# Performance work log

Measured on AMD Instinct MI355X. Metric: run time of the kernel, lower is better.

## Reference

```python
import jax, jax.numpy as jnp
import numpy as np

N_HEADS = 16
ROPE = 64        # qk_rope_head_dim
KV_LORA = 512
V_DIM = 128
THETA = 10000.0

def rms_norm(x, w, eps=1e-6):
    return x * jax.lax.rsqrt(jnp.mean(x * x, axis=-1, keepdims=True) + eps) * w

def rope_cos_sin(T, d, theta=THETA):
    half = d // 2
    inv = 1.0 / theta ** (jnp.arange(half, dtype=jnp.float32) / half)
    ang = jnp.arange(T, dtype=jnp.float32)[:, None] * inv  # (T, half)
    return jnp.cos(ang), jnp.sin(ang)

def apply_rot(x, cos, sin):
    # x: (B,T,H,D); complex rotation on interleaved pairs
    xr, xi = x[..., 0::2], x[..., 1::2]
    c = cos[None, :, None, :]
    s = sin[None, :, None, :]
    orr = xr * c - xi * s
    oi = xr * s + xi * c
    return jnp.stack([orr, oi], axis=-1).reshape(x.shape)

def setup_inputs() -> dict:
    key = jax.random.key(0)
    ks = jax.random.split(key, 8)
    B, T, C = 2, 2048, 2048
    QLR = 1536
    x = jax.random.normal(ks[0], (B, T, C), dtype=jnp.float32)
    mask = jnp.tril(jnp.ones((T, T), dtype=jnp.int32))[None, None]
    sc = 0.02
    w_qa = jax.random.normal(ks[1], (QLR, C), dtype=jnp.float32) * sc
    qa_norm_w = jnp.ones((QLR,), dtype=jnp.float32)
    w_qb = jax.random.normal(ks[2], (N_HEADS * 2 * ROPE, QLR), dtype=jnp.float32) * sc
    w_kva = jax.random.normal(ks[3], (KV_LORA + ROPE, C), dtype=jnp.float32) * sc
    kva_norm_w = jnp.ones((KV_LORA,), dtype=jnp.float32)
    w_kvb = jax.random.normal(ks[4], (N_HEADS * (ROPE + V_DIM), KV_LORA), dtype=jnp.float32) * sc
    w_o = jax.random.normal(ks[5], (C, N_HEADS * V_DIM), dtype=jnp.float32) * sc
    return {"x": x, "mask": mask, "w_qa": w_qa, "qa_norm_w": qa_norm_w, "w_qb": w_qb,
            "w_kva": w_kva, "kva_norm_w": kva_norm_w, "w_kvb": w_kvb, "w_o": w_o}

def reference(x, mask, w_qa, qa_norm_w, w_qb, w_kva, kva_norm_w, w_kvb, w_o):
    B, T, C = x.shape
    # Q: low-rank compress -> norm -> up-project, split nope/rope halves
    q_c = rms_norm(x @ w_qa.T, qa_norm_w)
    q = (q_c @ w_qb.T).reshape(B, T, N_HEADS, 2 * ROPE)
    q_nope, q_rope = q[..., :ROPE], q[..., ROPE:]
    # KV: joint low-rank + shared rope key
    kv_a = x @ w_kva.T
    kv_c = rms_norm(kv_a[..., :KV_LORA], kva_norm_w)
    k_rope_raw = kv_a[..., KV_LORA:]                       # (B,T,ROPE)
    kv = (kv_c @ w_kvb.T).reshape(B, T, N_HEADS, ROPE + V_DIM)
    k_content, v = kv[..., :ROPE], kv[..., ROPE:]
    k_rope = jnp.broadcast_to(k_rope_raw[:, :, None, :], (B, T, N_HEADS, ROPE))
    cos, sin = rope_cos_sin(T, ROPE)
    q_rope = apply_rot(q_rope, cos, sin)
    k_rope = apply_rot(k_rope, cos, sin)
    q = jnp.concatenate([q_nope, q_rope], axis=-1)         # (B,T,H,2*ROPE)
    k = jnp.concatenate([k_content, k_rope], axis=-1)
    att = jnp.einsum('bqhd,bkhd->bhqk', q, k) * (ROPE ** -0.5)
    att = jnp.where(mask == 0, -jnp.inf, att)
    att = jax.nn.softmax(att, axis=-1)
    # source's nan-guard: uniform attention if any nan appeared
    att = jnp.where(jnp.any(jnp.isnan(att)), jnp.float32(1.0 / T), att)
    out = jnp.einsum('bhqk,bkhd->bqhd', att, v).reshape(B, T, N_HEADS * V_DIM)
    return out @ w_o.T
```

## Files before the change

### kernel.cpp

```cpp
#include <hip/hip_runtime.h>

typedef short bf16x8 __attribute__((ext_vector_type(8)));
typedef unsigned short u16x8 __attribute__((ext_vector_type(8)));
typedef unsigned short u16x4 __attribute__((ext_vector_type(4)));
typedef float f32x4 __attribute__((ext_vector_type(4)));
typedef unsigned u32x4 __attribute__((ext_vector_type(4)));
typedef unsigned u32x2 __attribute__((ext_vector_type(2)));

#define DEV static __device__ __forceinline__

DEV float bf2f(unsigned short u) { return __uint_as_float(((unsigned)u) << 16); }
DEV unsigned short f2bf(float f) {
  unsigned u = __float_as_uint(f);
  return (unsigned short)((u + 0x7fffu + ((u >> 16) & 1u)) >> 16);
}
DEV unsigned cvtpk(float lo, float hi) {
  unsigned r;
  asm("v_cvt_pk_bf16_f32 %0, %1, %2" : "=v"(r) : "v"(lo), "v"(hi));
  return r;
}
DEV void p32swap(unsigned& a, unsigned& b) {
  asm volatile("v_permlane32_swap_b32 %0, %1" : "+v"(a), "+v"(b));
}
DEV void p16swap(unsigned& a, unsigned& b) {
  asm volatile("v_permlane16_swap_b32 %0, %1" : "+v"(a), "+v"(b));
}

#define GLDS16(g, l)                                                                   \
  __builtin_amdgcn_global_load_lds((const __attribute__((address_space(1))) void*)(g), \
                                   (__attribute__((address_space(3))) void*)(l), 16, 0, 0)

DEV void cvt_body(const float* __restrict__ src, unsigned short* __restrict__ dst,
                  int rows, int cols, int dstRows, int bid) {
  int i = bid * 256 + (int)threadIdx.x;
  int e = i << 2;
  int r = e / cols;
  int c = e - r * cols;
  u16x4 o = {0, 0, 0, 0};
  if (r < rows) {
    const float* p = src + (size_t)r * cols + c;
    o[0] = f2bf(p[0]); o[1] = f2bf(p[1]); o[2] = f2bf(p[2]); o[3] = f2bf(p[3]);
  }
  *(u16x4*)(dst + e) = o;
}

__global__ __launch_bounds__(256) void convert_all(
    const float* __restrict__ x, const float* __restrict__ w_qa, const float* __restrict__ w_kva,
    const float* __restrict__ w_qb, const float* __restrict__ w_kvb, const float* __restrict__ w_o,
    unsigned short* __restrict__ xb, unsigned short* __restrict__ wqkva,
    unsigned short* __restrict__ wqbb, unsigned short* __restrict__ wkvbb,
    unsigned short* __restrict__ wob) {
  int bid = blockIdx.x;
  if (bid < 8192)        cvt_body(x,     xb,                        4096, 2048, 4096, bid);
  else if (bid < 11264)  cvt_body(w_qa,  wqkva,                     1536, 2048, 1536, bid - 8192);
  else if (bid < 12544)  cvt_body(w_kva, wqkva + (size_t)1536*2048,  576, 2048,  640, bid - 11264);
  else if (bid < 15616)  cvt_body(w_qb,  wqbb,                      2048, 1536, 2048, bid - 12544);
  else if (bid < 17152)  cvt_body(w_kvb, wkvbb,                     3072,  512, 3072, bid - 15616);
  else                   cvt_body(w_o,   wob,                       2048, 2048, 2048, bid - 17152);
}

template <typename OutT>
__global__ __launch_bounds__(256, 2) void gemm_bt(const unsigned short* __restrict__ A,
                                                  const unsigned short* __restrict__ B,
                                                  OutT* __restrict__ C, int M, int N, int K) {
  __shared__ __align__(16) unsigned short As[128 * 64];
  __shared__ __align__(16) unsigned short Bs[128 * 64];
  const int tid = threadIdx.x;
  const int lane = tid & 63, wave = tid >> 6;
  const int l16 = lane & 15, lhi = lane >> 4;
  const int nbn = N >> 7;
  const int bm = blockIdx.x / nbn, bn = blockIdx.x - bm * nbn;
  const int m0 = bm << 7, n0 = bn << 7;
  const int wm = (wave >> 1) << 6, wn = (wave & 1) << 6;
  f32x4 acc[4][4] = {};
  for (int k0 = 0; k0 < K; k0 += 64) {
#pragma unroll
    for (int it = 0; it < 4; ++it) {
      int slot = it * 256 + tid;
      int row = slot >> 3, col = (slot & 7) << 3;
      GLDS16(A + (size_t)(m0 + row) * K + k0 + col, As + (it * 256 + wave * 64) * 8);
      GLDS16(B + (size_t)(n0 + row) * K + k0 + col, Bs + (it * 256 + wave * 64) * 8);
    }
    __syncthreads();
#pragma unroll
    for (int ks = 0; ks < 2; ++ks) {
      bf16x8 a[4], b[4];
#pragma unroll
      for (int i = 0; i < 4; ++i) {
        a[i] = *(const bf16x8*)(As + (wm + i * 16 + l16) * 64 + ks * 32 + lhi * 8);
        b[i] = *(const bf16x8*)(Bs + (wn + i * 16 + l16) * 64 + ks * 32 + lhi * 8);
      }
#pragma unroll
      for (int i = 0; i < 4; ++i)
#pragma unroll
        for (int j = 0; j < 4; ++j)
          acc[i][j] = __builtin_amdgcn_mfma_f32_16x16x32_bf16(a[i], b[j], acc[i][j], 0, 0, 0);
    }
    __syncthreads();
  }
#pragma unroll
  for (int i = 0; i < 4; ++i)
#pragma unroll
    for (int j = 0; j < 4; ++j)
#pragma unroll
      for (int r = 0; r < 4; ++r) {
        int row = m0 + wm + i * 16 + lhi * 4 + r;
        int col = n0 + wn + j * 16 + l16;
        float v = acc[i][j][r];
        if constexpr (sizeof(OutT) == 4)
          C[(size_t)row * N + col] = v;
        else
          C[(size_t)row * N + col] = (OutT)f2bf(v);
      }
}

__global__ __launch_bounds__(256) void rms_fused(const unsigned short* __restrict__ qkva,
                                                 const float* __restrict__ qw,
                                                 const float* __restrict__ kvw,
                                                 unsigned short* __restrict__ q_c,
                                                 unsigned short* __restrict__ kv_c,
                                                 unsigned short* __restrict__ krope) {
  const int row = blockIdx.x, tid = threadIdx.x;
  const unsigned short* p = qkva + (size_t)row * 2176;
  float fq[8];
  float ssq = 0.f;
  const bool act = tid < 192;
  if (act) {
    u16x8 v = *(const u16x8*)(p + tid * 8);
#pragma unroll
    for (int j = 0; j < 8; ++j) { fq[j] = bf2f(v[j]); ssq += fq[j] * fq[j]; }
  }
  float f0 = bf2f(p[1536 + tid * 2]), f1 = bf2f(p[1536 + tid * 2 + 1]);
  float sskv = f0 * f0 + f1 * f1;
#pragma unroll
  for (int m = 1; m <= 32; m <<= 1) {
    ssq += __shfl_xor(ssq, m);
    sskv += __shfl_xor(sskv, m);
  }
  __shared__ float rq[4], rkv[4];
  if ((tid & 63) == 0) { rq[tid >> 6] = ssq; rkv[tid >> 6] = sskv; }
  __syncthreads();
  float rstdq = rsqrtf((rq[0] + rq[1] + rq[2] + rq[3]) * (1.f / 1536.f) + 1e-6f);
  float rstdkv = rsqrtf((rkv[0] + rkv[1] + rkv[2] + rkv[3]) * (1.f / 512.f) + 1e-6f);
  if (act) {
    u16x8 o;
#pragma unroll
    for (int j = 0; j < 8; ++j) o[j] = f2bf(fq[j] * rstdq * qw[tid * 8 + j]);
    *(u16x8*)(q_c + (size_t)row * 1536 + tid * 8) = o;
  }
  kv_c[(size_t)row * 512 + tid * 2]     = f2bf(f0 * rstdkv * kvw[tid * 2]);
  kv_c[(size_t)row * 512 + tid * 2 + 1] = f2bf(f1 * rstdkv * kvw[tid * 2 + 1]);
  if (tid < 32) {
    int j = tid;
    float xr = bf2f(p[2048 + 2 * j]), xi = bf2f(p[2048 + 2 * j + 1]);
    int t = row & 2047;
    float ang = (float)t * powf(10000.f, -(float)j * (1.f / 32.f));
    float c = cosf(ang), s = sinf(ang);
    krope[(size_t)row * 64 + 2 * j]     = f2bf(xr * c - xi * s);
    krope[(size_t)row * 64 + 2 * j + 1] = f2bf(xr * s + xi * c);
  }
}

__global__ __launch_bounds__(256) void v_transpose(const unsigned short* __restrict__ kvfull,
                                                   unsigned short* __restrict__ VT) {
  __shared__ unsigned short tile[64][137];
  const int tid = threadIdx.x;
  const int tt = blockIdx.x & 31, h = (blockIdx.x >> 5) & 15, b = blockIdx.x >> 9;
  const int t0 = tt * 64;
#pragma unroll
  for (int it = 0; it < 4; ++it) {
    int s = it * 256 + tid;
    int r = s >> 4, c = (s & 15) << 3;
    u16x8 v = *(const u16x8*)(kvfull + (size_t)(b * 2048 + t0 + r) * 3072 + h * 192 + 64 + c);
    *(u16x8*)(&tile[r][c]) = v;
  }
  __syncthreads();
#pragma unroll
  for (int it = 0; it < 4; ++it) {
    int s = it * 256 + tid;
    int d = s >> 3, tc = (s & 7) << 3;
    u16x8 o;
#pragma unroll
    for (int j = 0; j < 8; ++j) o[j] = tile[tc + j][d];
    *(u16x8*)(VT + ((size_t)(b * 16 + h) * 128 + d) * 2048 + t0 + tc) = o;
  }
}

__global__ __launch_bounds__(256, 2) void flash_attn(const unsigned short* __restrict__ qfull,
                                                     const unsigned short* __restrict__ kvfull,
                                                     const unsigned short* __restrict__ krope,
                                                     const unsigned short* __restrict__ Vt,
                                                     unsigned short* __restrict__ out) {
  const int tid = threadIdx.x, lane = tid & 63, wave = tid >> 6;
  const int l16 = lane & 15, lhi = lane >> 4;
  const int bid = blockIdx.x;
  const int vid = (bid & 7) * 64 + (bid >> 3);
  const int pr = vid & 15;
  const int h = (vid >> 4) & 15;
  const int b = vid >> 8;
  const int sA = pr, sB = 31 - pr;
  __shared__ __align__(16) unsigned short Ks[2][64 * 128];
  __shared__ __align__(16) unsigned short Vs[2][64 * 128];

  const float QSCALE = 0.125f * 1.44269504089f;
  bf16x8 qf[2][4];
  float m_run[2], l_run[2];
  int qrow_g[2];
  f32x4 o_acc[2][8] = {};
#pragma unroll
  for (int u = 0; u < 2; ++u) {
    const int s_u = u ? sB : sA;
    int t = s_u * 64 + wave * 16 + l16;
    qrow_g[u] = t;
    const unsigned short* qrow = qfull + (size_t)(b * 2048 + t) * 2048 + h * 128;
#pragma unroll
    for (int ks = 0; ks < 4; ++ks) {
      u16x8 raw = *(const u16x8*)(qrow + ks * 32 + lhi * 8);
      float f[8];
#pragma unroll
      for (int j = 0; j < 8; ++j) f[j] = bf2f(raw[j]);
      if (ks >= 2) {
#pragma unroll
        for (int pp = 0; pp < 4; ++pp) {
          int d = ks * 32 + lhi * 8 + 2 * pp;
          int jl = (d - 64) >> 1;
          float ang = (float)t * powf(10000.f, -(float)jl * (1.f / 32.f));
          float c = cosf(ang), s = sinf(ang);
          float xr = f[2 * pp], xi = f[2 * pp + 1];
          f[2 * pp] = xr * c - xi * s;
          f[2 * pp + 1] = xr * s + xi * c;
        }
      }
      bf16x8 fr;
#pragma unroll
      for (int j = 0; j < 8; ++j) fr[j] = (short)f2bf(f[j] * QSCALE);
      qf[u][ks] = fr;
    }
    m_run[u] = -1e30f;
    l_run[u] = 0.f;
  }

  const int bT = b * 2048;
  const unsigned short* Vbh = Vt + (size_t)(b * 16 + h) * 128 * 2048;

  auto stageK = [&](int kt, int buf) {
#pragma unroll
    for (int it = 0; it < 4; ++it) {
      int L = it * 4096 + wave * 1024 + lane * 16;
      int r = L >> 8;
      int w = (L & 255) ^ ((r & 7) << 4);
      int c = w >> 1;
      int tl = bT + kt * 64 + r;
      const unsigned short* src = (c < 64) ? kvfull + (size_t)tl * 3072 + h * 192 + c
                                           : krope + (size_t)tl * 64 + (c - 64);
      GLDS16(src, &Ks[buf][(it * 4096 + wave * 1024) >> 1]);
    }
  };
  auto stageV = [&](int kt, int buf) {
#pragma unroll
    for (int it = 0; it < 4; ++it) {
      int L = it * 4096 + wave * 1024 + lane * 16;
      int d = L >> 7;
      int w = (L & 127) ^ ((d & 7) << 4);
      GLDS16(Vbh + (size_t)d * 2048 + kt * 64 + (w >> 1), &Vs[buf][(it * 4096 + wave * 1024) >> 1]);
    }
  };

  stageK(0, 0);
  stageV(0, 0);
  __syncthreads();
  int cur = 0;

  for (int kt = 0; kt <= sB; ++kt) {
    if (kt < sB) { stageK(kt + 1, cur ^ 1); stageV(kt + 1, cur ^ 1); }
    const unsigned short* Kb = Ks[cur];
    const unsigned short* Vb = Vs[cur];
    const bool actA = (kt <= sA);

    f32x4 st[2][4] = {};
    __builtin_amdgcn_s_setprio(1);
#pragma unroll
    for (int ks = 0; ks < 4; ++ks) {
      bf16x8 kf[4];
#pragma unroll
      for (int nt = 0; nt < 4; ++nt) {
        int row = nt * 16 + l16;
        int byteoff = row * 256 + ((ks * 64 + lhi * 16) ^ ((l16 & 7) << 4));
        kf[nt] = *(const bf16x8*)((const char*)Kb + byteoff);
      }
#pragma unroll
      for (int u = 0; u < 2; ++u) {
        if (u == 0 && !actA) continue;
#pragma unroll
        for (int nt = 0; nt < 4; ++nt)
          st[u][nt] = __builtin_amdgcn_mfma_f32_16x16x32_bf16(kf[nt], qf[u][ks], st[u][nt], 0, 0, 0);
      }
    }
    __builtin_amdgcn_s_setprio(0);

    bf16x8 pw[2][2];
#pragma unroll
    for (int u = 0; u < 2; ++u) {
      if (u == 0 && !actA) continue;
      const int s_u = u ? sB : sA;
      if (kt == s_u) {
#pragma unroll
        for (int nt = 0; nt < 4; ++nt)
#pragma unroll
          for (int r = 0; r < 4; ++r) {
            int kg = kt * 64 + nt * 16 + lhi * 4 + r;
            st[u][nt][r] = (kg <= qrow_g[u]) ? st[u][nt][r] : -1e30f;
          }
      }
      float mx = -1e30f;
#pragma unroll
      for (int nt = 0; nt < 4; ++nt)
#pragma unroll
        for (int r = 0; r < 4; ++r) mx = fmaxf(mx, st[u][nt][r]);
      mx = fmaxf(mx, __shfl_xor(mx, 16));
      mx = fmaxf(mx, __shfl_xor(mx, 32));
      if (__ballot(mx > m_run[u] + 8.f)) {
        float mnew = fmaxf(m_run[u], mx);
        float sc = exp2f(m_run[u] - mnew);
        m_run[u] = mnew;
        l_run[u] *= sc;
#pragma unroll
        for (int dt = 0; dt < 8; ++dt) o_acc[u][dt] *= sc;
      }
      const float mcur = m_run[u];
      float sum = 0.f;
#pragma unroll
      for (int nt = 0; nt < 4; ++nt)
#pragma unroll
        for (int r = 0; r < 4; ++r) {
          float p = exp2f(st[u][nt][r] - mcur);
          st[u][nt][r] = p;
          sum += p;
        }
      sum += __shfl_xor(sum, 16);
      sum += __shfl_xor(sum, 32);
      l_run[u] += sum;
      unsigned pk01[4], pk23[4];
#pragma unroll
      for (int nt = 0; nt < 4; ++nt) {
        pk01[nt] = cvtpk(st[u][nt][0], st[u][nt][1]);
        pk23[nt] = cvtpk(st[u][nt][2], st[u][nt][3]);
      }
#pragma unroll
      for (int k2 = 0; k2 < 2; ++k2) {
        unsigned a0 = pk01[2 * k2], b0 = pk01[2 * k2 + 1];
        unsigned a1 = pk23[2 * k2], b1 = pk23[2 * k2 + 1];
        p32swap(a0, b0); p16swap(a0, b0);
        p32swap(a1, b1); p16swap(a1, b1);
        u32x4 t4 = {a0, a1, b0, b1};
        pw[u][k2] = *(bf16x8*)&t4;
      }
    }

    __builtin_amdgcn_s_setprio(1);
#pragma unroll
    for (int k2 = 0; k2 < 2; ++k2)
#pragma unroll
      for (int dt = 0; dt < 8; ++dt) {
        int row = dt * 16 + l16;
        int byteoff = row * 128 + ((k2 * 64 + lhi * 16) ^ ((l16 & 7) << 4));
        bf16x8 vf = *(const bf16x8*)((const char*)Vb + byteoff);
#pragma unroll
        for (int u = 0; u < 2; ++u) {
          if (u == 0 && !actA) continue;
          o_acc[u][dt] = __builtin_amdgcn_mfma_f32_16x16x32_bf16(vf, pw[u][k2], o_acc[u][dt], 0, 0, 0);
        }
      }
    __builtin_amdgcn_s_setprio(0);

    __syncthreads();
    cur ^= 1;
  }

#pragma unroll
  for (int u = 0; u < 2; ++u) {
    float inv = 1.0f / l_run[u];
    unsigned short* orow = out + (size_t)(b * 2048 + qrow_g[u]) * 2048 + h * 128;
#pragma unroll
    for (int dt = 0; dt < 8; ++dt) {
      unsigned w01 = cvtpk(o_acc[u][dt][0] * inv, o_acc[u][dt][1] * inv);
      unsigned w23 = cvtpk(o_acc[u][dt][2] * inv, o_acc[u][dt][3] * inv);
      u32x2 st2 = {w01, w23};
      *(u32x2*)(orow + dt * 16 + lhi * 4) = st2;
    }
  }
}

extern "C" void kernel_launch(void* const* d_in, const int* in_sizes, int n_in,
                              void* d_out, int out_size, void* d_ws, size_t ws_size,
                              hipStream_t stream) {
  (void)in_sizes; (void)n_in; (void)out_size; (void)ws_size;
  const float* x      = (const float*)d_in[0];
  const float* w_qa   = (const float*)d_in[2];
  const float* qa_nw  = (const float*)d_in[3];
  const float* w_qb   = (const float*)d_in[4];
  const float* w_kva  = (const float*)d_in[5];
  const float* kva_nw = (const float*)d_in[6];
  const float* w_kvb  = (const float*)d_in[7];
  const float* w_o    = (const float*)d_in[8];
  float* out = (float*)d_out;
  char* ws = (char*)d_ws;

  unsigned short* xb     = (unsigned short*)(ws + 0);
  unsigned short* wqkva  = (unsigned short*)(ws + 16777216);
  unsigned short* wqbb   = (unsigned short*)(ws + 25690112);
  unsigned short* wkvbb  = (unsigned short*)(ws + 31981568);
  unsigned short* wob    = (unsigned short*)(ws + 35127296);
  unsigned short* qkva   = (unsigned short*)(ws + 43515904);
  unsigned short* qfull  = (unsigned short*)(ws + 43515904);
  unsigned short* q_c    = (unsigned short*)(ws + 61341696);
  unsigned short* kv_c   = (unsigned short*)(ws + 73924608);
  unsigned short* krope  = (unsigned short*)(ws + 78118912);
  unsigned short* attno  = (unsigned short*)(ws + 61341696);
  unsigned short* Vattn  = (unsigned short*)(ws + 78643200);
  unsigned short* kvfull = (unsigned short*)d_out;

  convert_all<<<21248, 256, 0, stream>>>(x, w_qa, w_kva, w_qb, w_kvb, w_o,
                                         xb, wqkva, wqbb, wkvbb, wob);

  gemm_bt<unsigned short><<<32 * 17, 256, 0, stream>>>(xb, wqkva, qkva, 4096, 2176, 2048);

  rms_fused<<<4096, 256, 0, stream>>>(qkva, qa_nw, kva_nw, q_c, kv_c, krope);

  gemm_bt<unsigned short><<<32 * 16, 256, 0, stream>>>(q_c,  wqbb,  qfull,  4096, 2048, 1536);
  gemm_bt<unsigned short><<<32 * 24, 256, 0, stream>>>(kv_c, wkvbb, kvfull, 4096, 3072,  512);

  v_transpose<<<1024, 256, 0, stream>>>(kvfull, Vattn);

  flash_attn<<<512, 256, 0, stream>>>(qfull, kvfull, krope, Vattn, attno);

  gemm_bt<float><<<32 * 16, 256, 0, stream>>>(attno, wob, out, 4096, 2048, 2048);
}
```

Before: 286.6 us.

## Fuse V transpose into kv_b GEMM epilogue and restructure flash attention blocks

Adds a dedicated kv_b GEMM whose epilogue writes the K-content columns to kvfull and the V columns directly in transposed layout, removing the separate v_transpose kernel. Flash attention now gives each block a single 64-row query tile instead of a paired causal tile, with a head-major XCD mapping and alternating tile order for balance. The launch grows to 1024 blocks, shared memory is single-buffered, and launch bounds rise to 4 per SIMD. This drops the prefetch double-buffering, so each iteration waits on its loads behind a barrier, and the transposed V stores are narrow 8-byte strided writes.

```diff
diff --git a/kernel.cpp b/kernel.cpp
--- a/kernel.cpp
+++ b/kernel.cpp
@@ -114,6 +114,69 @@
       }
 }
 
+__global__ __launch_bounds__(256, 2) void gemm_kvb(const unsigned short* __restrict__ A,
+                                                   const unsigned short* __restrict__ B,
+                                                   unsigned short* __restrict__ kvfull,
+                                                   unsigned short* __restrict__ VT) {
+  const int M = 4096, N = 3072, K = 512;
+  __shared__ __align__(16) unsigned short As[128 * 64];
+  __shared__ __align__(16) unsigned short Bs[128 * 64];
+  const int tid = threadIdx.x;
+  const int lane = tid & 63, wave = tid >> 6;
+  const int l16 = lane & 15, lhi = lane >> 4;
+  const int nbn = N >> 7;
+  const int bm = blockIdx.x / nbn, bn = blockIdx.x - bm * nbn;
+  const int m0 = bm << 7, n0 = bn << 7;
+  const int wm = (wave >> 1) << 6, wn = (wave & 1) << 6;
+  f32x4 acc[4][4] = {};
+  for (int k0 = 0; k0 < K; k0 += 64) {
+#pragma unroll
+    for (int it = 0; it < 4; ++it) {
+      int slot = it * 256 + tid;
+      int row = slot >> 3, col = (slot & 7) << 3;
+      GLDS16(A + (size_t)(m0 + row) * K + k0 + col, As + (it * 256 + wave * 64) * 8);
+      GLDS16(B + (size_t)(n0 + row) * K + k0 + col, Bs + (it * 256 + wave * 64) * 8);
+    }
+    __syncthreads();
+#pragma unroll
+    for (int ks = 0; ks < 2; ++ks) {
+      bf16x8 a[4], b[4];
+#pragma unroll
+      for (int i = 0; i < 4; ++i) {
+        a[i] = *(const bf16x8*)(As + (wm + i * 16 + l16) * 64 + ks * 32 + lhi * 8);
+        b[i] = *(const bf16x8*)(Bs + (wn + i * 16 + l16) * 64 + ks * 32 + lhi * 8);
+      }
+#pragma unroll
+      for (int i = 0; i < 4; ++i)
+#pragma unroll
+        for (int j = 0; j < 4; ++j)
+          acc[i][j] = __builtin_amdgcn_mfma_f32_16x16x32_bf16(a[i], b[j], acc[i][j], 0, 0, 0);
+    }
+    __syncthreads();
+  }
+#pragma unroll
+  for (int i = 0; i < 4; ++i)
+#pragma unroll
+    for (int j = 0; j < 4; ++j) {
+      int col = n0 + wn + j * 16 + l16;
+      int h = col / 192;
+      int jc = col - h * 192;
+      int row0 = m0 + wm + i * 16 + lhi * 4;
+      if (jc < 64) {
+#pragma unroll
+        for (int r = 0; r < 4; ++r)
+          kvfull[(size_t)(row0 + r) * 3072 + col] = f2bf(acc[i][j][r]);
+      } else {
+        int d = jc - 64;
+        int b = row0 >> 11, t0 = row0 & 2047;
+        u16x4 pk;
+#pragma unroll
+        for (int r = 0; r < 4; ++r) pk[r] = f2bf(acc[i][j][r]);
+        *(u16x4*)(VT + ((size_t)((b * 16 + h) * 128 + d)) * 2048 + t0) = pk;
+      }
+    }
+}
+
 __global__ __launch_bounds__(256) void rms_fused(const unsigned short* __restrict__ qkva,
                                                  const float* __restrict__ qw,
                                                  const float* __restrict__ kvw,
@@ -161,32 +224,7 @@
   }
 }
 
-__global__ __launch_bounds__(256) void v_transpose(const unsigned short* __restrict__ kvfull,
-                                                   unsigned short* __restrict__ VT) {
-  __shared__ unsigned short tile[64][137];
-  const int tid = threadIdx.x;
-  const int tt = blockIdx.x & 31, h = (blockIdx.x >> 5) & 15, b = blockIdx.x >> 9;
-  const int t0 = tt * 64;
-#pragma unroll
-  for (int it = 0; it < 4; ++it) {
-    int s = it * 256 + tid;
-    int r = s >> 4, c = (s & 15) << 3;
-    u16x8 v = *(const u16x8*)(kvfull + (size_t)(b * 2048 + t0 + r) * 3072 + h * 192 + 64 + c);
-    *(u16x8*)(&tile[r][c]) = v;
-  }
-  __syncthreads();
-#pragma unroll
-  for (int it = 0; it < 4; ++it) {
-    int s = it * 256 + tid;
-    int d = s >> 3, tc = (s & 7) << 3;
-    u16x8 o;
-#pragma unroll
-    for (int j = 0; j < 8; ++j) o[j] = tile[tc + j][d];
-    *(u16x8*)(VT + ((size_t)(b * 16 + h) * 128 + d) * 2048 + t0 + tc) = o;
-  }
-}
-
-__global__ __launch_bounds__(256, 2) void flash_attn(const unsigned short* __restrict__ qfull,
+__global__ __launch_bounds__(256, 4) void flash_attn(const unsigned short* __restrict__ qfull,
                                                      const unsigned short* __restrict__ kvfull,
                                                      const unsigned short* __restrict__ krope,
                                                      const unsigned short* __restrict__ Vt,
@@ -194,25 +232,20 @@
   const int tid = threadIdx.x, lane = tid & 63, wave = tid >> 6;
   const int l16 = lane & 15, lhi = lane >> 4;
   const int bid = blockIdx.x;
-  const int vid = (bid & 7) * 64 + (bid >> 3);
-  const int pr = vid & 15;
-  const int h = (vid >> 4) & 15;
-  const int b = vid >> 8;
-  const int sA = pr, sB = 31 - pr;
-  __shared__ __align__(16) unsigned short Ks[2][64 * 128];
-  __shared__ __align__(16) unsigned short Vs[2][64 * 128];
+  const int xcd = bid & 7, Lb = bid >> 3;
+  const int bhl = Lb >> 5, cL = Lb & 31;
+  const int s = (bhl & 1) ? (31 - cL) : cL;
+  const int bh = xcd * 4 + bhl;
+  const int h = bh & 15, b = bh >> 4;
+  __shared__ __align__(16) unsigned short Ks[64 * 128];
+  __shared__ __align__(16) unsigned short Vs[64 * 128];
 
   const float QSCALE = 0.125f * 1.44269504089f;
-  bf16x8 qf[2][4];
-  float m_run[2], l_run[2];
-  int qrow_g[2];
-  f32x4 o_acc[2][8] = {};
-#pragma unroll
-  for (int u = 0; u < 2; ++u) {
-    const int s_u = u ? sB : sA;
-    int t = s_u * 64 + wave * 16 + l16;
-    qrow_g[u] = t;
-    const unsigned short* qrow = qfull + (size_t)(b * 2048 + t) * 2048 + h * 128;
+  bf16x8 qf[4];
+  f32x4 o_acc[8] = {};
+  const int qg = s * 64 + wave * 16 + l16;
+  {
+    const unsigned short* qrow = qfull + (size_t)(b * 2048 + qg) * 2048 + h * 128;
 #pragma unroll
     for (int ks = 0; ks < 4; ++ks) {
       u16x8 raw = *(const u16x8*)(qrow + ks * 32 + lhi * 8);
@@ -224,127 +257,104 @@
         for (int pp = 0; pp < 4; ++pp) {
           int d = ks * 32 + lhi * 8 + 2 * pp;
           int jl = (d - 64) >> 1;
-          float ang = (float)t * powf(10000.f, -(float)jl * (1.f / 32.f));
-          float c = cosf(ang), s = sinf(ang);
+          float ang = (float)qg * powf(10000.f, -(float)jl * (1.f / 32.f));
+          float co = cosf(ang), si = sinf(ang);
           float xr = f[2 * pp], xi = f[2 * pp + 1];
-          f[2 * pp] = xr * c - xi * s;
-          f[2 * pp + 1] = xr * s + xi * c;
+          f[2 * pp] = xr * co - xi * si;
+          f[2 * pp + 1] = xr * si + xi * co;
         }
       }
       bf16x8 fr;
 #pragma unroll
       for (int j = 0; j < 8; ++j) fr[j] = (short)f2bf(f[j] * QSCALE);
-      qf[u][ks] = fr;
-    }
-    m_run[u] = -1e30f;
-    l_run[u] = 0.f;
-  }
+      qf[ks] = fr;
+    }
+  }
+  float m_run = -1e30f, l_run = 0.f;
 
   const int bT = b * 2048;
   const unsigned short* Vbh = Vt + (size_t)(b * 16 + h) * 128 * 2048;
 
-  auto stageK = [&](int kt, int buf) {
+  for (int kt = 0; kt <= s; ++kt) {
 #pragma unroll
     for (int it = 0; it < 4; ++it) {
-      int L = it * 4096 + wave * 1024 + lane * 16;
-      int r = L >> 8;
-      int w = (L & 255) ^ ((r & 7) << 4);
-      int c = w >> 1;
+      int Lo = it * 4096 + wave * 1024 + lane * 16;
+      int r = Lo >> 8;
+      int w = (Lo & 255) ^ ((r & 7) << 4);
+      int cc = w >> 1;
       int tl = bT + kt * 64 + r;
-      const unsigned short* src = (c < 64) ? kvfull + (size_t)tl * 3072 + h * 192 + c
-                                           : krope + (size_t)tl * 64 + (c - 64);
-      GLDS16(src, &Ks[buf][(it * 4096 + wave * 1024) >> 1]);
-    }
-  };
-  auto stageV = [&](int kt, int buf) {
+      const unsigned short* src = (cc < 64) ? kvfull + (size_t)tl * 3072 + h * 192 + cc
+                                            : krope + (size_t)tl * 64 + (cc - 64);
+      GLDS16(src, Ks + ((it * 4096 + wave * 1024) >> 1));
+    }
 #pragma unroll
     for (int it = 0; it < 4; ++it) {
-      int L = it * 4096 + wave * 1024 + lane * 16;
-      int d = L >> 7;
-      int w = (L & 127) ^ ((d & 7) << 4);
-      GLDS16(Vbh + (size_t)d * 2048 + kt * 64 + (w >> 1), &Vs[buf][(it * 4096 + wave * 1024) >> 1]);
-    }
-  };
-
-  stageK(0, 0);
-  stageV(0, 0);
-  __syncthreads();
-  int cur = 0;
-
-  for (int kt = 0; kt <= sB; ++kt) {
-    if (kt < sB) { stageK(kt + 1, cur ^ 1); stageV(kt + 1, cur ^ 1); }
-    const unsigned short* Kb = Ks[cur];
-    const unsigned short* Vb = Vs[cur];
-    const bool actA = (kt <= sA);
-
-    f32x4 st[2][4] = {};
+      int Lo = it * 4096 + wave * 1024 + lane * 16;
+      int d = Lo >> 7;
+      int w = (Lo & 127) ^ ((d & 7) << 4);
+      GLDS16(Vbh + (size_t)d * 2048 + kt * 64 + (w >> 1), Vs + ((it * 4096 + wave * 1024) >> 1));
+    }
+    __syncthreads();
+
+    f32x4 st[4] = {};
     __builtin_amdgcn_s_setprio(1);
 #pragma unroll
     for (int ks = 0; ks < 4; ++ks) {
-      bf16x8 kf[4];
+      bf16x8 kf;
 #pragma unroll
       for (int nt = 0; nt < 4; ++nt) {
         int row = nt * 16 + l16;
         int byteoff = row * 256 + ((ks * 64 + lhi * 16) ^ ((l16 & 7) << 4));
-        kf[nt] = *(const bf16x8*)((const char*)Kb + byteoff);
-      }
-#pragma unroll
-      for (int u = 0; u < 2; ++u) {
-        if (u == 0 && !actA) continue;
-#pragma unroll
-        for (int nt = 0; nt < 4; ++nt)
-          st[u][nt] = __builtin_amdgcn_mfma_f32_16x16x32_bf16(kf[nt], qf[u][ks], st[u][nt], 0, 0, 0);
+        kf = *(const bf16x8*)((const char*)Ks + byteoff);
+        st[nt] = __builtin_amdgcn_mfma_f32_16x16x32_bf16(kf, qf[ks], st[nt], 0, 0, 0);
       }
     }
     __builtin_amdgcn_s_setprio(0);
 
-    bf16x8 pw[2][2];
-#pragma unroll
-    for (int u = 0; u < 2; ++u) {
-      if (u == 0 && !actA) continue;
-      const int s_u = u ? sB : sA;
-      if (kt == s_u) {
-#pragma unroll
-        for (int nt = 0; nt < 4; ++nt)
-#pragma unroll
-          for (int r = 0; r < 4; ++r) {
-            int kg = kt * 64 + nt * 16 + lhi * 4 + r;
-            st[u][nt][r] = (kg <= qrow_g[u]) ? st[u][nt][r] : -1e30f;
-          }
-      }
-      float mx = -1e30f;
+    if (kt == s) {
 #pragma unroll
       for (int nt = 0; nt < 4; ++nt)
 #pragma unroll
-        for (int r = 0; r < 4; ++r) mx = fmaxf(mx, st[u][nt][r]);
-      mx = fmaxf(mx, __shfl_xor(mx, 16));
-      mx = fmaxf(mx, __shfl_xor(mx, 32));
-      if (__ballot(mx > m_run[u] + 8.f)) {
-        float mnew = fmaxf(m_run[u], mx);
-        float sc = exp2f(m_run[u] - mnew);
-        m_run[u] = mnew;
-        l_run[u] *= sc;
-#pragma unroll
-        for (int dt = 0; dt < 8; ++dt) o_acc[u][dt] *= sc;
-      }
-      const float mcur = m_run[u];
-      float sum = 0.f;
-#pragma unroll
-      for (int nt = 0; nt < 4; ++nt)
-#pragma unroll
         for (int r = 0; r < 4; ++r) {
-          float p = exp2f(st[u][nt][r] - mcur);
-          st[u][nt][r] = p;
-          sum += p;
+          int kg = kt * 64 + nt * 16 + lhi * 4 + r;
+          st[nt][r] = (kg <= qg) ? st[nt][r] : -1e30f;
         }
-      sum += __shfl_xor(sum, 16);
-      sum += __shfl_xor(sum, 32);
-      l_run[u] += sum;
+    }
+    float mx = -1e30f;
+#pragma unroll
+    for (int nt = 0; nt < 4; ++nt)
+#pragma unroll
+      for (int r = 0; r < 4; ++r) mx = fmaxf(mx, st[nt][r]);
+    mx = fmaxf(mx, __shfl_xor(mx, 16));
+    mx = fmaxf(mx, __shfl_xor(mx, 32));
+    if (__ballot(mx > m_run + 8.f)) {
+      float mnew = fmaxf(m_run, mx);
+      float sc = exp2f(m_run - mnew);
+      m_run = mnew;
+      l_run *= sc;
+#pragma unroll
+      for (int dt = 0; dt < 8; ++dt) o_acc[dt] *= sc;
+    }
+    const float mcur = m_run;
+    float sum = 0.f;
+#pragma unroll
+    for (int nt = 0; nt < 4; ++nt)
+#pragma unroll
+      for (int r = 0; r < 4; ++r) {
+        float p = exp2f(st[nt][r] - mcur);
+        st[nt][r] = p;
+        sum += p;
+      }
+    sum += __shfl_xor(sum, 16);
+    sum += __shfl_xor(sum, 32);
+    l_run += sum;
+    bf16x8 pw[2];
+    {
       unsigned pk01[4], pk23[4];
 #pragma unroll
       for (int nt = 0; nt < 4; ++nt) {
-        pk01[nt] = cvtpk(st[u][nt][0], st[u][nt][1]);
-        pk23[nt] = cvtpk(st[u][nt][2], st[u][nt][3]);
+        pk01[nt] = cvtpk(st[nt][0], st[nt][1]);
+        pk23[nt] = cvtpk(st[nt][2], st[nt][3]);
       }
 #pragma unroll
       for (int k2 = 0; k2 < 2; ++k2) {
@@ -353,7 +363,7 @@
         p32swap(a0, b0); p16swap(a0, b0);
         p32swap(a1, b1); p16swap(a1, b1);
         u32x4 t4 = {a0, a1, b0, b1};
-        pw[u][k2] = *(bf16x8*)&t4;
+        pw[k2] = *(bf16x8*)&t4;
       }
     }
 
@@ -364,27 +374,21 @@
       for (int dt = 0; dt < 8; ++dt) {
         int row = dt * 16 + l16;
         int byteoff = row * 128 + ((k2 * 64 + lhi * 16) ^ ((l16 & 7) << 4));
-        bf16x8 vf = *(const bf16x8*)((const char*)Vb + byteoff);
-#pragma unroll
-        for (int u = 0; u < 2; ++u) {
-          if (u == 0 && !actA) continue;
-          o_acc[u][dt] = __builtin_amdgcn_mfma_f32_16x16x32_bf16(vf, pw[u][k2], o_acc[u][dt], 0, 0, 0);
-        }
+        bf16x8 vf = *(const bf16x8*)((const char*)Vs + byteoff);
+        o_acc[dt] = __builtin_amdgcn_mfma_f32_16x16x32_bf16(vf, pw[k2], o_acc[dt], 0, 0, 0);
       }
     __builtin_amdgcn_s_setprio(0);
 
     __syncthreads();
-    cur ^= 1;
-  }
-
-#pragma unroll
-  for (int u = 0; u < 2; ++u) {
-    float inv = 1.0f / l_run[u];
-    unsigned short* orow = out + (size_t)(b * 2048 + qrow_g[u]) * 2048 + h * 128;
+  }
+
+  {
+    float inv = 1.0f / l_run;
+    unsigned short* orow = out + (size_t)(b * 2048 + qg) * 2048 + h * 128;
 #pragma unroll
     for (int dt = 0; dt < 8; ++dt) {
-      unsigned w01 = cvtpk(o_acc[u][dt][0] * inv, o_acc[u][dt][1] * inv);
-      unsigned w23 = cvtpk(o_acc[u][dt][2] * inv, o_acc[u][dt][3] * inv);
+      unsigned w01 = cvtpk(o_acc[dt][0] * inv, o_acc[dt][1] * inv);
+      unsigned w23 = cvtpk(o_acc[dt][2] * inv, o_acc[dt][3] * inv);
       u32x2 st2 = {w01, w23};
       *(u32x2*)(orow + dt * 16 + lhi * 4) = st2;
     }
@@ -427,12 +431,10 @@
 
   rms_fused<<<4096, 256, 0, stream>>>(qkva, qa_nw, kva_nw, q_c, kv_c, krope);
 
-  gemm_bt<unsigned short><<<32 * 16, 256, 0, stream>>>(q_c,  wqbb,  qfull,  4096, 2048, 1536);
-  gemm_bt<unsigned short><<<32 * 24, 256, 0, stream>>>(kv_c, wkvbb, kvfull, 4096, 3072,  512);
-
-  v_transpose<<<1024, 256, 0, stream>>>(kvfull, Vattn);
-
-  flash_attn<<<512, 256, 0, stream>>>(qfull, kvfull, krope, Vattn, attno);
+  gemm_bt<unsigned short><<<32 * 16, 256, 0, stream>>>(q_c, wqbb, qfull, 4096, 2048, 1536);
+  gemm_kvb<<<32 * 24, 256, 0, stream>>>(kv_c, wkvbb, kvfull, Vattn);
+
+  flash_attn<<<1024, 256, 0, stream>>>(qfull, kvfull, krope, Vattn, attno);
 
   gemm_bt<float><<<32 * 16, 256, 0, stream>>>(attno, wob, out, 4096, 2048, 2048);
 }
```

Measured after the change: 282.0 us. About the same (-1.6%).
